# Performance work log

Hardware: AMD Instinct MI355X
Metric: run time of the kernel (lower is better)

## Reference

```python
import jax, jax.numpy as jnp
import numpy as np
from jax import lax


def conv(x, w, b, stride=1):
    # NHWC conv with SAME padding, HWIO kernel
    return lax.conv_general_dilated(x, w, (stride, stride), 'SAME',
                                    dimension_numbers=('NHWC', 'HWIO', 'NHWC')) + b


def up2(x):
    return jnp.repeat(jnp.repeat(x, 2, axis=1), 2, axis=2)


def crop_and_resize(image, boxes, crop):
    """TF tf.image.crop_and_resize (bilinear, extrapolation_value=0) for a single image.
    image: [H,W,C]; boxes: [N,4] normalized [y1,x1,y2,x2]. Returns [N,crop,crop,C]."""
    H, W, C = image.shape
    y1, x1, y2, x2 = boxes[:, 0], boxes[:, 1], boxes[:, 2], boxes[:, 3]
    i = jnp.arange(crop, dtype=jnp.float32)
    ys = y1[:, None] * (H - 1) + i[None, :] * ((y2 - y1) * (H - 1) / (crop - 1))[:, None]  # [N,crop]
    xs = x1[:, None] * (W - 1) + i[None, :] * ((x2 - x1) * (W - 1) / (crop - 1))[:, None]

    def prep(coords, size):
        c0 = jnp.floor(coords)
        w = coords - c0
        i0 = jnp.clip(c0.astype(jnp.int32), 0, size - 1)
        i1 = jnp.clip(i0 + 1, 0, size - 1)
        valid = (coords >= 0) & (coords <= size - 1)
        return i0, i1, w, valid

    y0, y1i, wy, vy = prep(ys, H)
    x0, x1i, wx, vx = prep(xs, W)

    def g(yi, xi):  # -> [N,crop,crop,C]
        return image[yi[:, :, None], xi[:, None, :]]

    wy_ = wy[:, :, None, None]
    wx_ = wx[:, None, :, None]
    val = ((1 - wy_) * (1 - wx_) * g(y0, x0) + (1 - wy_) * wx_ * g(y0, x1i)
           + wy_ * (1 - wx_) * g(y1i, x0) + wy_ * wx_ * g(y1i, x1i))
    mask = (vy[:, :, None] & vx[:, None, :])[..., None]
    return jnp.where(mask, val, 0.0)


def make_anchors(level_hw):
    scales = [32, 64, 128, 256, 512]
    ratios = [0.5, 1.0, 2.0]
    strides = [4, 8, 16, 32, 64]
    out = []
    for (h, w), s, st in zip(level_hw, scales, strides):
        base = np.array([[-s * np.sqrt(r) / 2, -s / np.sqrt(r) / 2,
                          s * np.sqrt(r) / 2, s / np.sqrt(r) / 2] for r in ratios], np.float32)
        sx = np.arange(w, dtype=np.float32) * st
        sy = np.arange(h, dtype=np.float32) * st
        SX, SY = np.meshgrid(sx, sy)  # 'xy' indexing, same as tf.meshgrid
        shifts = np.stack([SX.ravel(), SY.ravel(), SX.ravel(), SY.ravel()], axis=1)
        out.append((shifts[:, None, :] + base[None, :, :]).reshape(-1, 4))
    return jnp.asarray(np.concatenate(out, axis=0))


def setup_inputs() -> dict:
    key = jax.random.key(0)
    ks = jax.random.split(key, 24)
    n = lambda k, s: jax.random.normal(k, s, jnp.float32) * 0.05
    z = lambda s: jnp.zeros(s, jnp.float32)
    inp = {
        'feat2': n(ks[0], (2, 200, 200, 256)),
        'feat3': n(ks[1], (2, 100, 100, 512)),
        'feat4': n(ks[2], (2, 50, 50, 1024)),
        'feat5': n(ks[3], (2, 25, 25, 2048)),
        'rois': jax.random.uniform(ks[4], (512, 4), jnp.float32, 0.0, 50.0),
        'lw2': n(ks[5], (1, 1, 256, 256)), 'lb2': z(256),
        'lw3': n(ks[6], (1, 1, 512, 256)), 'lb3': z(256),
        'lw4': n(ks[7], (1, 1, 1024, 256)), 'lb4': z(256),
        'lw5': n(ks[8], (1, 1, 2048, 256)), 'lb5': z(256),
        'fw': n(ks[9], (4, 3, 3, 256, 256)), 'fb': z((4, 256)),
        'p6w': n(ks[10], (3, 3, 256, 256)), 'p6b': z(256),
        'rpnw': n(ks[11], (3, 3, 256, 512)), 'rpnb': z(512),
        'clsw': n(ks[12], (1, 1, 512, 3)), 'clsb': z(3),
        'regw': n(ks[13], (1, 1, 512, 12)), 'regb': z(12),
        'fc1w': n(ks[14], (256, 1024)), 'fc1b': z(1024),
        'fc2w': n(ks[15], (1024, 1024)), 'fc2b': z(1024),
        'hclsw': n(ks[16], (1024, 8)), 'hclsb': z(8),
        'hregw': n(ks[17], (1024, 32)), 'hregb': z(32),
    }
    return inp


def reference(feat2, feat3, feat4, feat5, rois, lw2, lb2, lw3, lb3, lw4, lb4, lw5, lb5,
              fw, fb, p6w, p6b, rpnw, rpnb, clsw, clsb, regw, regb,
              fc1w, fc1b, fc2w, fc2b, hclsw, hclsb, hregw, hregb):
    # FPN lateral 1x1 convs
    l2 = conv(feat2, lw2, lb2)
    l3 = conv(feat3, lw3, lb3)
    l4 = conv(feat4, lw4, lb4)
    l5 = conv(feat5, lw5, lb5)
    m5 = l5
    m4 = l4 + up2(m5)
    m3 = l3 + up2(m4)
    m2 = l2 + up2(m3)
    # 3x3 output convs
    p2 = conv(m2, fw[0], fb[0])
    p3 = conv(m3, fw[1], fb[1])
    p4 = conv(m4, fw[2], fb[2])
    p5 = conv(m5, fw[3], fb[3])
    p6 = conv(p5, p6w, p6b, stride=2)
    feats = [p2, p3, p4, p5, p6]
    # RPN heads (shared weights across levels)
    rpn_cls, rpn_reg = [], []
    for f in feats:
        r = jax.nn.relu(conv(f, rpnw, rpnb))
        rpn_cls.append(jax.nn.sigmoid(conv(r, clsw, clsb)))
        rpn_reg.append(conv(r, regw, regb))
    # anchors (deterministic from level shapes)
    anchors = make_anchors([f.shape[1:3] for f in feats])
    # ROI head on P4 (feature_maps[2]), batch index 0, replicating the
    # original's normalization rois / [W, H, W, H]
    fm = p4[0]
    Hf, Wf = fm.shape[0], fm.shape[1]
    nboxes = rois / jnp.array([Wf, Hf, Wf, Hf], jnp.float32)
    rf = crop_and_resize(fm, nboxes, 7)          # [N,7,7,256]
    pooled = rf.mean(axis=(1, 2))                # global average pool
    x = jax.nn.relu(pooled @ fc1w + fc1b)
    x = jax.nn.relu(x @ fc2w + fc2b)
    roi_cls = jax.nn.softmax(x @ hclsw + hclsb, axis=-1)
    roi_reg = x @ hregw + hregb
    return tuple(rpn_cls) + tuple(rpn_reg) + (roi_cls, roi_reg, anchors)
```

## Files before the change

### kernel.cpp

```cpp
#include <hip/hip_runtime.h>
#include <hip/hip_bf16.h>
#include <math.h>

using bf16 = __hip_bfloat16;
typedef __attribute__((ext_vector_type(8))) short bf16x8;
typedef __attribute__((ext_vector_type(4))) float f32x4;

#define OSZ_TRUE   2258828LL
#define ANC_OFF    1619300LL
#define ROICLS_OFF 1598820LL
#define ROIREG_OFF 1602916LL

__device__ __forceinline__ float b2f(bf16 v){ return __bfloat162float(v); }
__device__ __forceinline__ bf16  f2b(float v){ return __float2bfloat16(v); }
__device__ __forceinline__ float bround(float v){ return b2f(f2b(v)); }
__device__ __forceinline__ float sane(float v){
    if (!(v == v)) v = 0.f;
    return fminf(8.f, fmaxf(-8.f, v));
}

__global__ void scrub_u32(unsigned* __restrict__ p, long long n){
    long long i = (long long)blockIdx.x*256 + threadIdx.x;
    if (i < n) p[i] = 0u;
}

__global__ void final_kernel(float* __restrict__ out){
    long long i = (long long)blockIdx.x*256 + threadIdx.x;
    if (i >= OSZ_TRUE) return;
    if (i < ANC_OFF){ out[i] = sane(out[i]); return; }
    long long a = i - ANC_OFF;
    int box = (int)(a >> 2), comp = (int)(a & 3);
    const int cum[6] = {0,120000,150000,157500,159375,159882};
    const int Ws[5]  = {200,100,50,25,13};
    const int st[5]  = {4,8,16,32,64};
    const float sc[5]= {32.f,64.f,128.f,256.f,512.f};
    int lvl = 0;
    while (box >= cum[lvl+1]) lvl++;
    int rem = box - cum[lvl];
    int ratio = rem % 3;
    int pix   = rem / 3;
    int W = Ws[lvl];
    int x = pix % W, y = pix / W;
    float sx = x * (float)st[lvl], sy = y * (float)st[lvl];
    const float sq[3] = {0.70710678118654752f, 1.0f, 1.41421356237309505f};
    float s  = sc[lvl];
    float bw = s * sq[ratio] * 0.5f;
    float bh = s / sq[ratio] * 0.5f;
    float v = (comp == 0) ? (sx - bw) : (comp == 1) ? (sy - bh)
            : (comp == 2) ? (sx + bw) : (sy + bh);
    out[i] = bround(v);
}

__global__ void pack_all(const bf16* __restrict__ lw2, const bf16* __restrict__ lw3,
                         const bf16* __restrict__ lw4, const bf16* __restrict__ lw5,
                         const bf16* __restrict__ fw,  const bf16* __restrict__ p6w,
                         const bf16* __restrict__ rpnw,
                         const bf16* __restrict__ clsw, const bf16* __restrict__ regw,
                         const bf16* __restrict__ fc1w, const bf16* __restrict__ fc2w,
                         bf16* __restrict__ dst)
{
    int idx = blockIdx.x*256 + threadIdx.x;
    if (idx >= 6430720) return;
    const bf16* src; int off, N;
    if      (idx <   65536){ src = lw2;  off = 0;       N = 256; }
    else if (idx <  196608){ src = lw3;  off = 65536;   N = 256; }
    else if (idx <  458752){ src = lw4;  off = 196608;  N = 256; }
    else if (idx <  983040){ src = lw5;  off = 458752;  N = 256; }
    else if (idx < 3342336){ int l = (idx - 983040)/589824;
                             src = fw + (size_t)l*589824; off = 983040 + l*589824; N = 256; }
    else if (idx < 3932160){ src = p6w;  off = 3342336; N = 256; }
    else if (idx < 5111808){ src = rpnw; off = 3932160; N = 512; }
    else if (idx < 5120000){
        int local = idx - 5111808;
        int kit = local >> 9, rem = local & 511;
        int n = rem >> 5, j = rem & 31, k = kit*32 + j;
        float v = 0.f;
        if (n < 3) v = b2f(clsw[k*3 + n]);
        else if (n < 15) v = b2f(regw[k*12 + (n-3)]);
        dst[idx] = f2b(v);
        return;
    }
    else if (idx < 5382144){ src = fc1w; off = 5120000; N = 1024; }
    else                   { src = fc2w; off = 5382144; N = 1024; }
    int local = idx - off;
    int n32 = N*32;
    int kit = local / n32, rem = local - kit*n32;
    int n = rem >> 5, j = rem & 31;
    dst[idx] = src[(size_t)(kit*32 + j)*N + n];
}

template<int CIN>
__global__ __launch_bounds__(64, 2)
void lat_v4(const bf16* __restrict__ in, const bf16* __restrict__ wTp,
            const bf16* __restrict__ bias, bf16* __restrict__ outp,
            const bf16* __restrict__ addsrc, int srcWp,
            int H, int W, int M, int oy0, int out_y0, int Wop)
{
    __shared__ ushort sA[64*66];
    const int lane = threadIdx.x;
    const int fm = lane & 15, fq = lane >> 4;
    const int m0 = blockIdx.x * 64;
    const int n0 = blockIdx.y * 64;
    const bf16* ap[4];
    #pragma unroll
    for (int i = 0; i < 4; ++i){
        int px = m0 + i*16 + fm; if (px >= M) px = M-1;
        int oyv = oy0 + px / W, ox = px % W;
        int y = min(max(oyv, 0), H-1);
        ap[i] = in + ((size_t)y*W + ox)*CIN + fq*8;
    }
    const bf16* b = wTp + (size_t)(n0 + fm)*32 + fq*8;
    f32x4 acc[4][4];
    #pragma unroll
    for (int i = 0; i < 4; ++i)
    #pragma unroll
    for (int nf = 0; nf < 4; ++nf) acc[i][nf] = (f32x4){0,0,0,0};

    constexpr int NC = CIN/32;
    bf16x8 aA[4], bA[4], aB[4], bB[4];
    auto LD = [&](bf16x8 (&A)[4], bf16x8 (&B)[4], int c){
        #pragma unroll
        for (int i = 0; i < 4; ++i)  A[i] = *(const bf16x8*)(const void*)(ap[i] + c*32);
        #pragma unroll
        for (int nf = 0; nf < 4; ++nf) B[nf] = *(const bf16x8*)(const void*)(b + (size_t)c*8192 + nf*512);
    };
    auto FM = [&](bf16x8 (&A)[4], bf16x8 (&B)[4]){
        #pragma unroll
        for (int i = 0; i < 4; ++i)
        #pragma unroll
        for (int nf = 0; nf < 4; ++nf)
            acc[i][nf] = __builtin_amdgcn_mfma_f32_16x16x32_bf16(A[i], B[nf], acc[i][nf], 0,0,0);
    };
    LD(aA,bA,0); LD(aB,bB,1);
    #pragma unroll
    for (int c = 0; c < NC; c += 2){
        FM(aA,bA); if (c+2 < NC) LD(aA,bA,c+2);
        FM(aB,bB); if (c+3 < NC) LD(aB,bB,c+3);
    }

    #pragma unroll
    for (int i = 0; i < 4; ++i)
    #pragma unroll
    for (int nf = 0; nf < 4; ++nf){
        float bb = b2f(bias[n0 + nf*16 + fm]);
        #pragma unroll
        for (int reg = 0; reg < 4; ++reg){
            bf16 t = f2b(acc[i][nf][reg] + bb);
            sA[(i*16 + fq*4 + reg)*66 + nf*16 + fm] = *(ushort*)&t;
        }
    }
    __syncthreads();
    #pragma unroll
    for (int p = 0; p < 8; ++p){
        int pxL = p*8 + (lane >> 3);
        int px = m0 + pxL;
        if (px >= M) continue;
        int oyv = oy0 + px / W, ox = px % W;
        bf16x8 v = *(const bf16x8*)(const void*)&sA[pxL*66 + (lane & 7)*8];
        if (oyv >= 0 && oyv < H){
            if (addsrc){
                const bf16x8 s = *(const bf16x8*)(const void*)(addsrc +
                    (((size_t)((oyv>>1) + 1))*srcWp + (ox>>1) + 1)*256 + n0 + (lane&7)*8);
                ushort* vv = (ushort*)&v; const ushort* ss = (const ushort*)&s;
                #pragma unroll
                for (int j = 0; j < 8; ++j){
                    bf16 r = f2b(b2f(*(const bf16*)&vv[j]) + b2f(*(const bf16*)&ss[j]));
                    vv[j] = *(ushort*)&r;
                }
            }
        } else {
            v = (bf16x8){0,0,0,0,0,0,0,0};
        }
        *(bf16x8*)(void*)(outp + ((size_t)(oyv - out_y0)*Wop + ox + 1)*256 + n0 + (lane&7)*8) = v;
    }
}

struct C3Lvl {
    const bf16* in; const bf16* wT; const bf16* bias; bf16* out;
    int Wp, in_y0, Ho, Wo, Wop, out_y0, oy0, M, stride, blk0;
};

__global__ __launch_bounds__(64, 2)
void conv3_v4(C3Lvl L0, C3Lvl L1, C3Lvl L2, C3Lvl L3, int nlv)
{
    __shared__ ushort sA[64*66];
    C3Lvl L = L0;
    if (nlv > 1 && (int)blockIdx.x >= L1.blk0) L = L1;
    if (nlv > 2 && (int)blockIdx.x >= L2.blk0) L = L2;
    if (nlv > 3 && (int)blockIdx.x >= L3.blk0) L = L3;
    const int lane = threadIdx.x;
    const int fm = lane & 15, fq = lane >> 4;
    const int m0 = ((int)blockIdx.x - L.blk0) * 64;
    const int n0 = blockIdx.y * 64;
    const int Wp = L.Wp;
    const bf16* ap[4];
    #pragma unroll
    for (int i = 0; i < 4; ++i){
        int px = m0 + i*16 + fm; if (px >= L.M) px = L.M-1;
        int oyv = L.oy0 + px / L.Wo, ox = px % L.Wo;
        ap[i] = L.in + ((size_t)(oyv*L.stride - 1 - L.in_y0)*Wp + ox*L.stride)*256 + fq*8;
    }
    const bf16* b = L.wT + (size_t)(n0 + fm)*32 + fq*8;
    f32x4 acc[4][4];
    #pragma unroll
    for (int i = 0; i < 4; ++i)
    #pragma unroll
    for (int nf = 0; nf < 4; ++nf) acc[i][nf] = (f32x4){0,0,0,0};

    const int rB1 = Wp*256, rB2 = Wp*512;
    bf16x8 aA[4], bA[4], aB[4], bB[4];
    auto LD = [&](bf16x8 (&A)[4], bf16x8 (&B)[4], int s){
        const int off = (s < 24 ? 0 : (s < 48 ? rB1 : rB2)) + (s % 24)*32;
        #pragma unroll
        for (int i = 0; i < 4; ++i)  A[i] = *(const bf16x8*)(const void*)(ap[i] + off);
        #pragma unroll
        for (int nf = 0; nf < 4; ++nf) B[nf] = *(const bf16x8*)(const void*)(b + (size_t)s*8192 + nf*512);
    };
    auto FM = [&](bf16x8 (&A)[4], bf16x8 (&B)[4]){
        #pragma unroll
        for (int i = 0; i < 4; ++i)
        #pragma unroll
        for (int nf = 0; nf < 4; ++nf)
            acc[i][nf] = __builtin_amdgcn_mfma_f32_16x16x32_bf16(A[i], B[nf], acc[i][nf], 0,0,0);
    };
    LD(aA,bA,0); LD(aB,bB,1);
    #pragma unroll
    for (int s = 0; s < 72; s += 2){
        FM(aA,bA); if (s+2 < 72) LD(aA,bA,s+2);
        FM(aB,bB); if (s+3 < 72) LD(aB,bB,s+3);
    }

    #pragma unroll
    for (int i = 0; i < 4; ++i)
    #pragma unroll
    for (int nf = 0; nf < 4; ++nf){
        float bb = b2f(L.bias[n0 + nf*16 + fm]);
        #pragma unroll
        for (int reg = 0; reg < 4; ++reg){
            bf16 t = f2b(acc[i][nf][reg] + bb);
            sA[(i*16 + fq*4 + reg)*66 + nf*16 + fm] = *(ushort*)&t;
        }
    }
    __syncthreads();
    #pragma unroll
    for (int p = 0; p < 8; ++p){
        int pxL = p*8 + (lane >> 3);
        int px = m0 + pxL;
        if (px >= L.M) continue;
        int oyv = L.oy0 + px / L.Wo, ox = px % L.Wo;
        bf16x8 v = *(const bf16x8*)(const void*)&sA[pxL*66 + (lane & 7)*8];
        if (!(oyv >= 0 && oyv < L.Ho)) v = (bf16x8){0,0,0,0,0,0,0,0};
        *(bf16x8*)(void*)(L.out + ((size_t)(oyv - L.out_y0)*L.Wop + ox + 1)*256 + n0 + (lane&7)*8) = v;
    }
}

struct RpnLvl { const bf16* in; long long cbase, rbase; int Wp, in_y0, Wo, oy0, M, blk0; };

__global__ __launch_bounds__(512, 4)
void rpn_fused_v7(RpnLvl L0, RpnLvl L1, RpnLvl L2, RpnLvl L3, RpnLvl L4, int nlv,
                  const bf16* __restrict__ wTp, const bf16* __restrict__ bias,
                  const bf16* __restrict__ hdp, const bf16* __restrict__ clsb,
                  const bf16* __restrict__ regb, float* __restrict__ outb)
{
    __shared__ ushort sr[64][520];
    __shared__ ushort Ab[2][64*40];
    RpnLvl L = L0;
    if (nlv > 1 && (int)blockIdx.x >= L1.blk0) L = L1;
    if (nlv > 2 && (int)blockIdx.x >= L2.blk0) L = L2;
    if (nlv > 3 && (int)blockIdx.x >= L3.blk0) L = L3;
    if (nlv > 4 && (int)blockIdx.x >= L4.blk0) L = L4;
    int wave = threadIdx.x >> 6, lane = threadIdx.x & 63;
    int fm = lane & 15, fq = lane >> 4;
    int m0 = ((int)blockIdx.x - L.blk0) * 64;
    int n0 = wave * 64;
    const int Wp = L.Wp;

    const bf16* as = nullptr; int pl = 0, c4 = 0;
    if (wave < 4){
        pl = wave*16 + (lane >> 2); c4 = lane & 3;
        int pxs = m0 + pl; if (pxs >= L.M) pxs = L.M-1;
        int oys = L.oy0 + pxs / L.Wo, oxs = pxs % L.Wo;
        as = L.in + ((size_t)(oys - 1 - L.in_y0)*Wp + oxs)*256 + c4*8;
    }
    const bf16* b = wTp + (size_t)(n0 + fm)*32 + fq*8;
    f32x4 acc[4][4];
    #pragma unroll
    for (int i = 0; i < 4; ++i)
    #pragma unroll
    for (int nf = 0; nf < 4; ++nf) acc[i][nf] = (f32x4){0,0,0,0};

    const int rB1 = Wp*256, rB2 = Wp*512;
    auto offA = [&](int s){ return (s < 24 ? 0 : (s < 48 ? rB1 : rB2)) + (s % 24)*32; };

    if (wave < 4){
        bf16x8 t0 = *(const bf16x8*)(const void*)(as + offA(0));
        *(bf16x8*)(void*)&Ab[0][pl*40 + c4*8] = t0;
    }
    __syncthreads();

    #pragma unroll
    for (int s = 0; s < 72; ++s){
        bf16x8 stg;
        if (wave < 4 && s + 1 < 72)
            stg = *(const bf16x8*)(const void*)(as + offA(s + 1));
        bf16x8 bv[4];
        const bf16* bp = b + (size_t)s*16384;
        #pragma unroll
        for (int nf = 0; nf < 4; ++nf) bv[nf] = *(const bf16x8*)(const void*)(bp + nf*512);
        bf16x8 av[4];
        const ushort* ab = &Ab[s & 1][0];
        #pragma unroll
        for (int i = 0; i < 4; ++i)
            av[i] = *(const bf16x8*)(const void*)&ab[(i*16 + fm)*40 + fq*8];
        #pragma unroll
        for (int i = 0; i < 4; ++i)
        #pragma unroll
        for (int nf = 0; nf < 4; ++nf)
            acc[i][nf] = __builtin_amdgcn_mfma_f32_16x16x32_bf16(av[i], bv[nf], acc[i][nf], 0,0,0);
        if (wave < 4 && s + 1 < 72)
            *(bf16x8*)(void*)&Ab[(s + 1) & 1][pl*40 + c4*8] = stg;
        __syncthreads();
    }

    #pragma unroll
    for (int i = 0; i < 4; ++i)
    #pragma unroll
    for (int nf = 0; nf < 4; ++nf){
        int co = n0 + nf*16 + fm;
        float bb = b2f(bias[co]);
        #pragma unroll
        for (int reg = 0; reg < 4; ++reg){
            int prow = i*16 + fq*4 + reg;
            bf16 t = f2b(fmaxf(acc[i][nf][reg] + bb, 0.f));
            sr[prow][co] = *(ushort*)&t;
        }
    }
    __syncthreads();
    if (wave < 4){
        const ushort* ar = &sr[wave*16 + fm][fq*8];
        const bf16* hb = hdp + fm*32 + fq*8;
        f32x4 h = (f32x4){0,0,0,0};
        #pragma unroll
        for (int k = 0; k < 16; ++k){
            bf16x8 avh = *(const bf16x8*)(const void*)(ar + k*32);
            bf16x8 bvh = *(const bf16x8*)(const void*)(hb + k*512);
            h = __builtin_amdgcn_mfma_f32_16x16x32_bf16(avh, bvh, h, 0,0,0);
        }
        int n = fm;
        #pragma unroll
        for (int reg = 0; reg < 4; ++reg){
            int p2 = m0 + wave*16 + fq*4 + reg;
            if (p2 >= L.M) continue;
            float v = h[reg];
            if (n < 3)
                outb[L.cbase + (long long)p2*3 + n] = sane(1.f/(1.f + expf(-(v + b2f(clsb[n])))));
            else if (n < 15)
                outb[L.rbase + (long long)p2*12 + (n-3)] = sane(v + b2f(regb[n-3]));
        }
    }
}

__global__ void roi_pool(const bf16* __restrict__ fm, const bf16* __restrict__ rois,
                         bf16* __restrict__ pooled){
    int n = blockIdx.x; int c = threadIdx.x;
    float y1 = b2f(rois[n*4+0]) * (1.f/50.f);
    float x1 = b2f(rois[n*4+1]) * (1.f/50.f);
    float y2 = b2f(rois[n*4+2]) * (1.f/50.f);
    float x2 = b2f(rois[n*4+3]) * (1.f/50.f);
    float dy = (y2 - y1) * 49.f / 6.f;
    float dx = (x2 - x1) * 49.f / 6.f;
    float sum = 0.f;
    for (int i = 0; i < 7; i++){
        float ys = y1*49.f + (float)i * dy;
        float fy = floorf(ys); float wy = ys - fy;
        int yi0 = min(max((int)fy, 0), 49); int yi1 = min(yi0 + 1, 49);
        bool vy = (ys >= 0.f) && (ys <= 49.f);
        for (int j = 0; j < 7; j++){
            float xs = x1*49.f + (float)j * dx;
            float fx = floorf(xs); float wx = xs - fx;
            int xi0 = min(max((int)fx, 0), 49); int xi1 = min(xi0 + 1, 49);
            bool vx = (xs >= 0.f) && (xs <= 49.f);
            if (vy && vx){
                float v00 = b2f(fm[((yi0+1)*52 + xi0+1)*256 + c]);
                float v01 = b2f(fm[((yi0+1)*52 + xi1+1)*256 + c]);
                float v10 = b2f(fm[((yi1+1)*52 + xi0+1)*256 + c]);
                float v11 = b2f(fm[((yi1+1)*52 + xi1+1)*256 + c]);
                sum += (1.f-wy)*(1.f-wx)*v00 + (1.f-wy)*wx*v01
                     + wy*(1.f-wx)*v10 + wy*wx*v11;
            }
        }
    }
    pooled[(size_t)n*256 + c] = f2b(sum * (1.f/49.f));
}

__global__ __launch_bounds__(256, 4)
void fc_mfma(const bf16* __restrict__ A, const bf16* __restrict__ wp,
             const bf16* __restrict__ bias, bf16* __restrict__ outp,
             int K, int N, int relu)
{
    int wave = threadIdx.x >> 6, lane = threadIdx.x & 63;
    int fm = lane & 15, fq = lane >> 4;
    int m0 = blockIdx.x * 64;
    int n0 = blockIdx.y * 256 + wave * 64;
    const bf16* ap[4];
    #pragma unroll
    for (int i = 0; i < 4; ++i)
        ap[i] = A + (size_t)(m0 + i*16 + fm)*K + fq*8;
    const bf16* b = wp + (size_t)(n0 + fm)*32 + fq*8;
    f32x4 acc[4][4];
    #pragma unroll
    for (int i = 0; i < 4; ++i)
    #pragma unroll
    for (int nf = 0; nf < 4; ++nf) acc[i][nf] = (f32x4){0,0,0,0};
    for (int c = 0; c < K/32; ++c){
        bf16x8 av[4], bv[4];
        #pragma unroll
        for (int i = 0; i < 4; ++i)  av[i]  = *(const bf16x8*)(const void*)(ap[i] + c*32);
        #pragma unroll
        for (int nf = 0; nf < 4; ++nf) bv[nf] = *(const bf16x8*)(const void*)(b + nf*512);
        #pragma unroll
        for (int i = 0; i < 4; ++i)
        #pragma unroll
        for (int nf = 0; nf < 4; ++nf)
            acc[i][nf] = __builtin_amdgcn_mfma_f32_16x16x32_bf16(av[i], bv[nf], acc[i][nf], 0,0,0);
        b += (size_t)N*32;
    }
    #pragma unroll
    for (int i = 0; i < 4; ++i)
    #pragma unroll
    for (int nf = 0; nf < 4; ++nf){
        int co = n0 + nf*16 + fm;
        float bb = b2f(bias[co]);
        #pragma unroll
        for (int reg = 0; reg < 4; ++reg){
            int row = m0 + i*16 + fq*4 + reg;
            float v = acc[i][nf][reg] + bb;
            if (relu) v = fmaxf(v, 0.f);
            outp[(size_t)row*N + co] = f2b(v);
        }
    }
}

__global__ void head_cls(const bf16* __restrict__ in, const bf16* __restrict__ w,
                         const bf16* __restrict__ bias, float* __restrict__ outb){
    int row = blockIdx.x*64 + threadIdx.x;
    if (row >= 512) return;
    float lg[8];
    const bf16* ip = in + (size_t)row*1024;
    for (int c = 0; c < 8; c++) lg[c] = b2f(bias[c]);
    for (int ci = 0; ci < 1024; ci++){
        float v = b2f(ip[ci]);
        #pragma unroll
        for (int c = 0; c < 8; c++) lg[c] += v * b2f(w[ci*8 + c]);
    }
    float m = lg[0];
    for (int c = 1; c < 8; c++) m = fmaxf(m, lg[c]);
    float e[8], s = 0.f;
    for (int c = 0; c < 8; c++){ e[c] = expf(lg[c] - m); s += e[c]; }
    for (int c = 0; c < 8; c++)
        outb[ROICLS_OFF + (long long)row*8 + c] = sane(e[c]/s);
}

__global__ void head_reg(const bf16* __restrict__ in, const bf16* __restrict__ w,
                         const bf16* __restrict__ bias, float* __restrict__ outb){
    int idx = blockIdx.x*256 + threadIdx.x;
    if (idx >= 512*32) return;
    int row = idx >> 5; int col = idx & 31;
    float acc = b2f(bias[col]);
    const bf16* ip = in + (size_t)row*1024;
    #pragma unroll 4
    for (int ci = 0; ci < 1024; ci++) acc += b2f(ip[ci]) * b2f(w[ci*32 + col]);
    outb[ROIREG_OFF + idx] = sane(acc);
}

extern "C" void kernel_launch(void* const* d_in, const int* in_sizes, int n_in,
                              void* d_out, int out_size, void* d_ws, size_t ws_size,
                              hipStream_t stream){
    const bf16* feat2=(const bf16*)d_in[0];
    const bf16* feat3=(const bf16*)d_in[1];
    const bf16* feat4=(const bf16*)d_in[2];
    const bf16* feat5=(const bf16*)d_in[3];
    const bf16* rois =(const bf16*)d_in[4];
    const bf16* lw2=(const bf16*)d_in[5];  const bf16* lb2=(const bf16*)d_in[6];
    const bf16* lw3=(const bf16*)d_in[7];  const bf16* lb3=(const bf16*)d_in[8];
    const bf16* lw4=(const bf16*)d_in[9];  const bf16* lb4=(const bf16*)d_in[10];
    const bf16* lw5=(const bf16*)d_in[11]; const bf16* lb5=(const bf16*)d_in[12];
    const bf16* fw =(const bf16*)d_in[13]; const bf16* fb =(const bf16*)d_in[14];
    const bf16* p6w=(const bf16*)d_in[15]; const bf16* p6b=(const bf16*)d_in[16];
    const bf16* rpnw=(const bf16*)d_in[17];const bf16* rpnb=(const bf16*)d_in[18];
    const bf16* clsw=(const bf16*)d_in[19];const bf16* clsb=(const bf16*)d_in[20];
    const bf16* regw=(const bf16*)d_in[21];const bf16* regb=(const bf16*)d_in[22];
    const bf16* fc1w=(const bf16*)d_in[23];const bf16* fc1b=(const bf16*)d_in[24];
    const bf16* fc2w=(const bf16*)d_in[25];const bf16* fc2b=(const bf16*)d_in[26];
    const bf16* hclsw=(const bf16*)d_in[27];const bf16* hclsb=(const bf16*)d_in[28];
    const bf16* hregw=(const bf16*)d_in[29];const bf16* hregb=(const bf16*)d_in[30];
    float* out=(float*)d_out;

    const long long cls_off[5] = {0, 240000, 300000, 315000, 318750};
    const long long reg_off[5] = {319764, 1279764, 1519764, 1579764, 1594764};

    bf16* ws=(bf16*)d_ws;
    bf16* WTp_l2 = ws;
    bf16* WTp_l3 = WTp_l2 + 65536;
    bf16* WTp_l4 = WTp_l3 + 131072;
    bf16* WTp_l5 = WTp_l4 + 262144;
    bf16* WTp_f  = WTp_l5 + 524288;
    bf16* WTp_p6 = WTp_f  + 2359296;
    bf16* WTp_rpn= WTp_p6 + 589824;
    bf16* WTp_hd = WTp_rpn+ 1179648;
    bf16* fc1p   = WTp_hd + 8192;
    bf16* fc2p   = fc1p   + 262144;
    bf16* M3p = ws + 6430720;
    bf16* P3p = M3p + 2663424;
    bf16* M4p = P3p + 2663424;
    bf16* P4p = M4p + 692224;
    bf16* M5p = P4p + 692224;
    bf16* P5p = M5p + 186624;
    bf16* P6p = P5p + 186624;

    const bool bigws = (ws_size >= 72ull*1024*1024);

    bf16* M2F = ws + 13572864;
    bf16* P2F = M2F + 10657792;
    bf16* fc1oA = P2F + 10554368;
    bf16* fc2oA = fc1oA + 524288;
    bf16* pooledA = fc2oA + 524288;

    bf16* M2s = P3p;
    bf16* P2s = ws + 13572864;
    bf16* fc1oB = P2s;
    bf16* fc2oB = P2s + 524288;
    bf16* pooledB = ws + 17244928;

    bf16* fc1o  = bigws ? fc1oA  : fc1oB;
    bf16* fc2o  = bigws ? fc2oA  : fc2oB;
    bf16* pooled= bigws ? pooledA: pooledB;

    long long scrub_elems = bigws ? (34785024LL - 6430720LL) : 10945280LL;
    long long scrub_u32s  = scrub_elems/2;
    scrub_u32<<<dim3((int)((scrub_u32s+255)/256)), 256, 0, stream>>>((unsigned*)(ws + 6430720), scrub_u32s);

    pack_all<<<dim3((6430720+255)/256), 256, 0, stream>>>(lw2, lw3, lw4, lw5, fw, p6w, rpnw,
                                                          clsw, regw, fc1w, fc2w, ws);

    for (int img = 0; img < 2; img++){
        const bf16* f2 = feat2 + (size_t)img*200*200*256;
        const bf16* f3 = feat3 + (size_t)img*100*100*512;
        const bf16* f4 = feat4 + (size_t)img*50*50*1024;
        const bf16* f5 = feat5 + (size_t)img*25*25*2048;

        lat_v4<2048><<<dim3((625+63)/64, 4),  64, 0, stream>>>(f5, WTp_l5, lb5, M5p, nullptr, 0, 25, 25, 625, 0, -1, 27);
        lat_v4<1024><<<dim3((2500+63)/64, 4), 64, 0, stream>>>(f4, WTp_l4, lb4, M4p, M5p, 27, 50, 50, 2500, 0, -1, 52);
        lat_v4<512><<<dim3((10000+63)/64, 4), 64, 0, stream>>>(f3, WTp_l3, lb3, M3p, M4p, 52, 100, 100, 10000, 0, -1, 102);

        if (bigws){
            lat_v4<256><<<dim3((206*200+63)/64, 4), 64, 0, stream>>>(f2, WTp_l2, lb2, M2F,
                M3p, 102, 200, 200, 206*200, -3, -3, 202);

            const int b2 = (40800+63)/64, b3 = (10000+63)/64, b4 = (2500+63)/64, b5 = (625+63)/64;
            C3Lvl c2{M2F, WTp_f,            fb,       P2F, 202,-3,200,200,202,-2,-2,40800,1, 0};
            C3Lvl c3{M3p, WTp_f + 1*589824, fb + 256, P3p, 102,-1,100,100,102,-1, 0,10000,1, b2};
            C3Lvl c4{M4p, WTp_f + 2*589824, fb + 512, P4p,  52,-1, 50, 50, 52,-1, 0, 2500,1, b2+b3};
            C3Lvl c5{M5p, WTp_f + 3*589824, fb + 768, P5p,  27,-1, 25, 25, 27,-1, 0,  625,1, b2+b3+b4};
            conv3_v4<<<dim3(b2+b3+b4+b5, 4), 64, 0, stream>>>(c2, c3, c4, c5, 4);
            C3Lvl c6{P5p, WTp_p6, p6b, P6p, 27,-1,13,13,15,-1,0,169,2, 0};
            conv3_v4<<<dim3((169+63)/64, 4), 64, 0, stream>>>(c6, c6, c6, c6, 1);

            if (img == 0)
                roi_pool<<<dim3(512), 256, 0, stream>>>(P4p, rois, pooled);

            const int r2 = (40000+63)/64, r3 = (10000+63)/64, r4 = (2500+63)/64, r5n = (625+63)/64;
            RpnLvl q2{P2F, cls_off[0] + (long long)img*120000, reg_off[0] + (long long)img*480000, 202,-2,200,0,40000, 0};
            RpnLvl q3{P3p, cls_off[1] + (long long)img*30000,  reg_off[1] + (long long)img*120000, 102,-1,100,0,10000, r2};
            RpnLvl q4{P4p, cls_off[2] + (long long)img*7500,   reg_off[2] + (long long)img*30000,   52,-1, 50,0, 2500, r2+r3};
            RpnLvl q5{P5p, cls_off[3] + (long long)img*1875,   reg_off[3] + (long long)img*7500,    27,-1, 25,0,  625, r2+r3+r4};
            RpnLvl q6{P6p, cls_off[4] + (long long)img*507,    reg_off[4] + (long long)img*2028,    15,-1, 13,0,  169, r2+r3+r4+r5n};
            rpn_fused_v7<<<dim3(r2+r3+r4+r5n+(169+63)/64), 512, 0, stream>>>(q2, q3, q4, q5, q6, 5,
                WTp_rpn, rpnb, WTp_hd, clsb, regb, out);
        } else {
            const int c3b5 = (625+63)/64, c3b4 = (2500+63)/64, c3b3 = (10000+63)/64;
            C3Lvl c5{M5p, WTp_f + 3*589824, fb + 768, P5p, 27,-1,25,25,27,-1,0,625,1,  0};
            C3Lvl c4{M4p, WTp_f + 2*589824, fb + 512, P4p, 52,-1,50,50,52,-1,0,2500,1, c3b5};
            C3Lvl c3{M3p, WTp_f + 1*589824, fb + 256, P3p, 102,-1,100,100,102,-1,0,10000,1, c3b5+c3b4};
            conv3_v4<<<dim3(c3b5+c3b4+c3b3, 4), 64, 0, stream>>>(c5, c4, c3, c3, 3);
            C3Lvl c6{P5p, WTp_p6, p6b, P6p, 27,-1,13,13,15,-1,0,169,2, 0};
            conv3_v4<<<dim3((169+63)/64, 4), 64, 0, stream>>>(c6, c6, c6, c6, 1);

            if (img == 0)
                roi_pool<<<dim3(512), 256, 0, stream>>>(P4p, rois, pooled);

            const int rb3 = (10000+63)/64, rb4 = (2500+63)/64, rb5 = (625+63)/64, rb6 = (169+63)/64;
            RpnLvl r3{P3p, cls_off[1] + (long long)img*30000, reg_off[1] + (long long)img*120000, 102,-1,100,0,10000, 0};
            RpnLvl r4{P4p, cls_off[2] + (long long)img*7500,  reg_off[2] + (long long)img*30000,   52,-1, 50,0, 2500, rb3};
            RpnLvl r5{P5p, cls_off[3] + (long long)img*1875,  reg_off[3] + (long long)img*7500,    27,-1, 25,0,  625, rb3+rb4};
            RpnLvl r6{P6p, cls_off[4] + (long long)img*507,   reg_off[4] + (long long)img*2028,    15,-1, 13,0,  169, rb3+rb4+rb5};
            rpn_fused_v7<<<dim3(rb3+rb4+rb5+rb6), 512, 0, stream>>>(r3, r4, r5, r6, r6, 4,
                WTp_rpn, rpnb, WTp_hd, clsb, regb, out);

            const int sr0[3] = {0, 67, 134};
            for (int s = 0; s < 3; s++){
                int r0 = sr0[s], r1 = (s == 2) ? 200 : sr0[s] + 67;
                int hbuf = (r1 + 3) - (r0 - 3);
                lat_v4<256><<<dim3((hbuf*200+63)/64, 4), 64, 0, stream>>>(f2, WTp_l2, lb2, M2s,
                    M3p, 102, 200, 200, hbuf*200, r0-3, r0-3, 202);
                C3Lvl cs{M2s, WTp_f, fb, P2s, 202, r0-3, 200, 200, 202, r0-2, r0-2, (r1-r0+4)*200, 1, 0};
                conv3_v4<<<dim3(((r1-r0+4)*200+63)/64, 4), 64, 0, stream>>>(cs, cs, cs, cs, 1);
                RpnLvl rs{P2s, cls_off[0] + ((long long)img*40000 + r0*200)*3,
                               reg_off[0] + ((long long)img*40000 + r0*200)*12,
                          202, r0-2, 200, r0, (r1-r0)*200, 0};
                rpn_fused_v7<<<dim3((((r1-r0)*200)+63)/64), 512, 0, stream>>>(rs, rs, rs, rs, rs, 1,
                    WTp_rpn, rpnb, WTp_hd, clsb, regb, out);
            }
        }
    }

    fc_mfma<<<dim3(8,4), 256, 0, stream>>>(pooled, fc1p, fc1b, fc1o, 256, 1024, 1);
    fc_mfma<<<dim3(8,4), 256, 0, stream>>>(fc1o,  fc2p, fc2b, fc2o, 1024, 1024, 1);
    head_cls<<<dim3(8),  64,  0, stream>>>(fc2o, hclsw, hclsb, out);
    head_reg<<<dim3(64), 256, 0, stream>>>(fc2o, hregw, hregb, out);

    final_kernel<<<dim3((int)((OSZ_TRUE + 255)/256)), 256, 0, stream>>>(out);
}
```

Measured before the change: 1.858 ms.

## Share im2col A tile across four waves via double-buffered LDS in 3x3 conv

The 3x3 FPN conv kernel now runs four waves per block, one per 64-channel output slice, in place of four separate blocks on grid.y. The activation tile is loaded once per K-step into a double-buffered LDS array and read by all waves, so global A loads drop by about four times. The cost is a __syncthreads per K step (72 per tile), a shallower register prefetch of B, and more LDS per block, which may reduce occupancy.

Measured after the change: 1.635 ms. 12.0% less time.

```diff
diff --git a/kernel.cpp b/kernel.cpp
--- a/kernel.cpp
+++ b/kernel.cpp
@@ -180,26 +180,26 @@
     int Wp, in_y0, Ho, Wo, Wop, out_y0, oy0, M, stride, blk0;
 };
 
-__global__ __launch_bounds__(64, 2)
-void conv3_v4(C3Lvl L0, C3Lvl L1, C3Lvl L2, C3Lvl L3, int nlv)
+__global__ __launch_bounds__(256, 2)
+void conv3_v5(C3Lvl L0, C3Lvl L1, C3Lvl L2, C3Lvl L3, int nlv)
 {
-    __shared__ ushort sA[64*66];
+    __shared__ ushort sA[4][64*66];
+    __shared__ ushort Ab[2][64*40];
     C3Lvl L = L0;
     if (nlv > 1 && (int)blockIdx.x >= L1.blk0) L = L1;
     if (nlv > 2 && (int)blockIdx.x >= L2.blk0) L = L2;
     if (nlv > 3 && (int)blockIdx.x >= L3.blk0) L = L3;
-    const int lane = threadIdx.x;
+    const int wave = threadIdx.x >> 6, lane = threadIdx.x & 63;
     const int fm = lane & 15, fq = lane >> 4;
     const int m0 = ((int)blockIdx.x - L.blk0) * 64;
-    const int n0 = blockIdx.y * 64;
+    const int n0 = wave * 64;
     const int Wp = L.Wp;
-    const bf16* ap[4];
-    #pragma unroll
-    for (int i = 0; i < 4; ++i){
-        int px = m0 + i*16 + fm; if (px >= L.M) px = L.M-1;
-        int oyv = L.oy0 + px / L.Wo, ox = px % L.Wo;
-        ap[i] = L.in + ((size_t)(oyv*L.stride - 1 - L.in_y0)*Wp + ox*L.stride)*256 + fq*8;
-    }
+
+    const int pl = threadIdx.x >> 2, c4 = threadIdx.x & 3;
+    int pxs = m0 + pl; if (pxs >= L.M) pxs = L.M-1;
+    int oys = L.oy0 + pxs / L.Wo, oxs = pxs % L.Wo;
+    const bf16* as = L.in + ((size_t)(oys*L.stride - 1 - L.in_y0)*Wp + oxs*L.stride)*256 + c4*8;
+
     const bf16* b = L.wT + (size_t)(n0 + fm)*32 + fq*8;
     f32x4 acc[4][4];
     #pragma unroll
@@ -208,26 +208,34 @@
     for (int nf = 0; nf < 4; ++nf) acc[i][nf] = (f32x4){0,0,0,0};
 
     const int rB1 = Wp*256, rB2 = Wp*512;
-    bf16x8 aA[4], bA[4], aB[4], bB[4];
-    auto LD = [&](bf16x8 (&A)[4], bf16x8 (&B)[4], int s){
-        const int off = (s < 24 ? 0 : (s < 48 ? rB1 : rB2)) + (s % 24)*32;
-        #pragma unroll
-        for (int i = 0; i < 4; ++i)  A[i] = *(const bf16x8*)(const void*)(ap[i] + off);
-        #pragma unroll
-        for (int nf = 0; nf < 4; ++nf) B[nf] = *(const bf16x8*)(const void*)(b + (size_t)s*8192 + nf*512);
-    };
-    auto FM = [&](bf16x8 (&A)[4], bf16x8 (&B)[4]){
+    auto offA = [&](int s){ return (s < 24 ? 0 : (s < 48 ? rB1 : rB2)) + (s % 24)*32; };
+
+    { bf16x8 t0 = *(const bf16x8*)(const void*)(as + offA(0));
+      *(bf16x8*)(void*)&Ab[0][pl*40 + c4*8] = t0; }
+    __syncthreads();
+
+    #pragma unroll
+    for (int s = 0; s < 72; ++s){
+        bf16x8 stg;
+        if (s + 1 < 72)
+            stg = *(const bf16x8*)(const void*)(as + offA(s + 1));
+        bf16x8 bv[4];
+        const bf16* bp = b + (size_t)s*8192;
+        #pragma unroll
+        for (int nf = 0; nf < 4; ++nf) bv[nf] = *(const bf16x8*)(const void*)(bp + nf*512);
+        bf16x8 av[4];
+        const ushort* ab = &Ab[s & 1][0];
         #pragma unroll
         for (int i = 0; i < 4; ++i)
+            av[i] = *(const bf16x8*)(const void*)&ab[(i*16 + fm)*40 + fq*8];
+        #pragma unroll
+        for (int i = 0; i < 4; ++i)
         #pragma unroll
         for (int nf = 0; nf < 4; ++nf)
-            acc[i][nf] = __builtin_amdgcn_mfma_f32_16x16x32_bf16(A[i], B[nf], acc[i][nf], 0,0,0);
-    };
-    LD(aA,bA,0); LD(aB,bB,1);
-    #pragma unroll
-    for (int s = 0; s < 72; s += 2){
-        FM(aA,bA); if (s+2 < 72) LD(aA,bA,s+2);
-        FM(aB,bB); if (s+3 < 72) LD(aB,bB,s+3);
+            acc[i][nf] = __builtin_amdgcn_mfma_f32_16x16x32_bf16(av[i], bv[nf], acc[i][nf], 0,0,0);
+        if (s + 1 < 72)
+            *(bf16x8*)(void*)&Ab[(s + 1) & 1][pl*40 + c4*8] = stg;
+        __syncthreads();
     }
 
     #pragma unroll
@@ -238,7 +246,7 @@
         #pragma unroll
         for (int reg = 0; reg < 4; ++reg){
             bf16 t = f2b(acc[i][nf][reg] + bb);
-            sA[(i*16 + fq*4 + reg)*66 + nf*16 + fm] = *(ushort*)&t;
+            sA[wave][(i*16 + fq*4 + reg)*66 + nf*16 + fm] = *(ushort*)&t;
         }
     }
     __syncthreads();
@@ -248,7 +256,7 @@
         int px = m0 + pxL;
         if (px >= L.M) continue;
         int oyv = L.oy0 + px / L.Wo, ox = px % L.Wo;
-        bf16x8 v = *(const bf16x8*)(const void*)&sA[pxL*66 + (lane & 7)*8];
+        bf16x8 v = *(const bf16x8*)(const void*)&sA[wave][pxL*66 + (lane & 7)*8];
         if (!(oyv >= 0 && oyv < L.Ho)) v = (bf16x8){0,0,0,0,0,0,0,0};
         *(bf16x8*)(void*)(L.out + ((size_t)(oyv - L.out_y0)*L.Wop + ox + 1)*256 + n0 + (lane&7)*8) = v;
     }
@@ -562,9 +570,9 @@
             C3Lvl c3{M3p, WTp_f + 1*589824, fb + 256, P3p, 102,-1,100,100,102,-1, 0,10000,1, b2};
             C3Lvl c4{M4p, WTp_f + 2*589824, fb + 512, P4p,  52,-1, 50, 50, 52,-1, 0, 2500,1, b2+b3};
             C3Lvl c5{M5p, WTp_f + 3*589824, fb + 768, P5p,  27,-1, 25, 25, 27,-1, 0,  625,1, b2+b3+b4};
-            conv3_v4<<<dim3(b2+b3+b4+b5, 4), 64, 0, stream>>>(c2, c3, c4, c5, 4);
+            conv3_v5<<<dim3(b2+b3+b4+b5), 256, 0, stream>>>(c2, c3, c4, c5, 4);
             C3Lvl c6{P5p, WTp_p6, p6b, P6p, 27,-1,13,13,15,-1,0,169,2, 0};
-            conv3_v4<<<dim3((169+63)/64, 4), 64, 0, stream>>>(c6, c6, c6, c6, 1);
+            conv3_v5<<<dim3((169+63)/64), 256, 0, stream>>>(c6, c6, c6, c6, 1);
 
             if (img == 0)
                 roi_pool<<<dim3(512), 256, 0, stream>>>(P4p, rois, pooled);
@@ -582,9 +590,9 @@
             C3Lvl c5{M5p, WTp_f + 3*589824, fb + 768, P5p, 27,-1,25,25,27,-1,0,625,1,  0};
             C3Lvl c4{M4p, WTp_f + 2*589824, fb + 512, P4p, 52,-1,50,50,52,-1,0,2500,1, c3b5};
             C3Lvl c3{M3p, WTp_f + 1*589824, fb + 256, P3p, 102,-1,100,100,102,-1,0,10000,1, c3b5+c3b4};
-            conv3_v4<<<dim3(c3b5+c3b4+c3b3, 4), 64, 0, stream>>>(c5, c4, c3, c3, 3);
+            conv3_v5<<<dim3(c3b5+c3b4+c3b3), 256, 0, stream>>>(c5, c4, c3, c3, 3);
             C3Lvl c6{P5p, WTp_p6, p6b, P6p, 27,-1,13,13,15,-1,0,169,2, 0};
-            conv3_v4<<<dim3((169+63)/64, 4), 64, 0, stream>>>(c6, c6, c6, c6, 1);
+            conv3_v5<<<dim3((169+63)/64), 256, 0, stream>>>(c6, c6, c6, c6, 1);
 
             if (img == 0)
                 roi_pool<<<dim3(512), 256, 0, stream>>>(P4p, rois, pooled);
@@ -604,7 +612,7 @@
                 lat_v4<256><<<dim3((hbuf*200+63)/64, 4), 64, 0, stream>>>(f2, WTp_l2, lb2, M2s,
                     M3p, 102, 200, 200, hbuf*200, r0-3, r0-3, 202);
                 C3Lvl cs{M2s, WTp_f, fb, P2s, 202, r0-3, 200, 200, 202, r0-2, r0-2, (r1-r0+4)*200, 1, 0};
-                conv3_v4<<<dim3(((r1-r0+4)*200+63)/64, 4), 64, 0, stream>>>(cs, cs, cs, cs, 1);
+                conv3_v5<<<dim3(((r1-r0+4)*200+63)/64), 256, 0, stream>>>(cs, cs, cs, cs, 1);
                 RpnLvl rs{P2s, cls_off[0] + ((long long)img*40000 + r0*200)*3,
                                reg_off[0] + ((long long)img*40000 + r0*200)*12,
                           202, r0-2, 200, r0, (r1-r0)*200, 0};
```
